# Kernel tuning notes

Measured on AMD Instinct MI355X. Metric: run time of the kernel, lower is better.

The kernel has to match this reference:

```python
import jax, jax.numpy as jnp
import numpy as np

D_MODEL = 1024
NUM_HEADS = 16
DEPTH = D_MODEL // NUM_HEADS
B, S = 2, 2048


def setup_inputs() -> dict:
    key = jax.random.key(0)
    ks = jax.random.split(key, 12)
    scale = 1.0 / np.sqrt(D_MODEL)
    inp = {
        "Q": jax.random.normal(ks[0], (B, S, D_MODEL), jnp.float32),
        "K": jax.random.normal(ks[1], (B, S, D_MODEL), jnp.float32),
        "V": jax.random.normal(ks[2], (B, S, D_MODEL), jnp.float32),
        # causal mask: 1 where attention is disallowed (strictly upper triangular)
        "mask": jnp.triu(jnp.ones((1, 1, S, S), jnp.float32), k=1),
        "Wq": jax.random.normal(ks[3], (D_MODEL, D_MODEL), jnp.float32) * scale,
        "bq": jnp.zeros((D_MODEL,), jnp.float32),
        "Wk": jax.random.normal(ks[4], (D_MODEL, D_MODEL), jnp.float32) * scale,
        "bk": jnp.zeros((D_MODEL,), jnp.float32),
        "Wv": jax.random.normal(ks[5], (D_MODEL, D_MODEL), jnp.float32) * scale,
        "bv": jnp.zeros((D_MODEL,), jnp.float32),
        "Wo": jax.random.normal(ks[6], (D_MODEL, D_MODEL), jnp.float32) * scale,
        "bo": jnp.zeros((D_MODEL,), jnp.float32),
    }
    return inp


def _split_heads(x):
    # [B, S, d_model] -> [B, H, S, depth]
    b, s, _ = x.shape
    return x.reshape(b, s, NUM_HEADS, DEPTH).transpose(0, 2, 1, 3)


def reference(Q, K, V, mask, Wq, bq, Wk, bk, Wv, bv, Wo, bo):
    q = _split_heads(Q @ Wq + bq)  # [B,H,S,depth]
    k = _split_heads(K @ Wk + bk)
    v = _split_heads(V @ Wv + bv)

    scale = 1.0 / jnp.sqrt(jnp.asarray(DEPTH, q.dtype))
    scores = jnp.einsum("bhqd,bhkd->bhqk", q, k) * scale
    scores = scores + mask * (-1e9)
    attn = jax.nn.softmax(scores, axis=-1)  # [B,H,S,S]
    ctx = jnp.einsum("bhqk,bhkd->bhqd", attn, v)

    # combine heads: [B,H,S,depth] -> [B,S,d_model]
    ctx = ctx.transpose(0, 2, 1, 3).reshape(Q.shape[0], -1, D_MODEL)
    out = ctx @ Wo + bo
    return out, attn
```

## Files before the change

### kernel.cpp

```cpp
#include <hip/hip_runtime.h>
#include <hip/hip_bf16.h>
#include <cstdint>
#include <cstddef>


typedef __bf16 bf16x8 __attribute__((ext_vector_type(8)));
typedef float  f32x4  __attribute__((ext_vector_type(4)));
typedef unsigned short u16;
typedef unsigned int   u32;

using gas_p = const __attribute__((address_space(1))) void*;
using las_p = __attribute__((address_space(3))) void*;

static __device__ __forceinline__ u16 f2bf(float x) {
    unsigned u = __builtin_bit_cast(unsigned, x);
    u += 0x7FFFu + ((u >> 16) & 1u);
    return (u16)(u >> 16);
}
static __device__ __forceinline__ u32 pk2(float a, float b) {
    return (u32)f2bf(a) | ((u32)f2bf(b) << 16);
}
static __device__ __forceinline__ f32x4 mfma16(bf16x8 a, bf16x8 b, f32x4 c) {
    return __builtin_amdgcn_mfma_f32_16x16x32_bf16(a, b, c, 0, 0, 0);
}
static __device__ __forceinline__ bf16x8 ldb8(const u16* p) {
    return *reinterpret_cast<const bf16x8*>(p);
}

__global__ __launch_bounds__(256) void transpose_cvt_k(const float* __restrict__ Wq,
                                                       const float* __restrict__ Wk,
                                                       const float* __restrict__ Wv,
                                                       const float* __restrict__ Wo,
                                                       u16* __restrict__ Wt3,
                                                       u16* __restrict__ Wto) {
    const int z = blockIdx.z;
    const float* in = (z == 0) ? Wq : (z == 1) ? Wk : (z == 2) ? Wv : Wo;
    u16* out = (z < 3) ? (Wt3 + (size_t)z * 1048576) : Wto;
    __shared__ float t[32][33];
    const int tx = threadIdx.x, ty = threadIdx.y;
    const int x  = blockIdx.x * 32 + tx;
    const int y0 = blockIdx.y * 32 + ty;
#pragma unroll
    for (int j = 0; j < 32; j += 8)
        t[ty + j][tx] = in[(size_t)(y0 + j) * 1024 + x];
    __syncthreads();
    const int x2 = blockIdx.y * 32 + tx;
    const int y2 = blockIdx.x * 32 + ty;
#pragma unroll
    for (int j = 0; j < 32; j += 8)
        out[(size_t)(y2 + j) * 1024 + x2] = f2bf(t[tx][ty + j]);
}

__global__ __launch_bounds__(256) void gemm_qkv_k(const float* __restrict__ Qf,
                                                  const float* __restrict__ Kf,
                                                  const float* __restrict__ Vf,
                                                  const u16* __restrict__ Wt3,
                                                  const float* __restrict__ bq,
                                                  const float* __restrict__ bk,
                                                  const float* __restrict__ bv,
                                                  u16* __restrict__ qf,
                                                  u16* __restrict__ kf,
                                                  u16* __restrict__ vtf,
                                                  float* __restrict__ attn) {
    constexpr int Kd = 1024;
    constexpr int S = 2048;
    const int z = blockIdx.z;

    if (z == 3) {
        float* attn_h = attn + (size_t)blockIdx.y * S * S;
        const int bx = blockIdx.x;
        const int ro = threadIdx.x >> 4, cc = threadIdx.x & 15;
        const f32x4 zz = {0.f, 0.f, 0.f, 0.f};
        for (int c = 1; c < 32; ++c) {
            float* base = attn_h + (size_t)(bx * 8 * c) * S + c * 64 + cc * 4;
            const int nrows = 8 * c;
            for (int i = ro; i < nrows; i += 16)
                *reinterpret_cast<f32x4*>(base + (size_t)i * S) = zz;
        }
        return;
    }

    const float* Af = (z == 0) ? Qf : (z == 1) ? Kf : Vf;
    const u16* Bt = Wt3 + (size_t)z * 1048576;
    const float* bias = (z == 0) ? bq : (z == 1) ? bk : bv;

    __shared__ __align__(16) u16 As[128 * 64];
    __shared__ __align__(16) u16 Bs[128 * 64];
    const int tid = threadIdx.x;
    const int w = tid >> 6, lane = tid & 63;
    const int g = lane >> 4, lr = lane & 15;
    const int wr = w >> 1, wc = w & 1;
    const int bm = blockIdx.y * 128, bn = blockIdx.x * 128;

    f32x4 acc[4][4];
#pragma unroll
    for (int a = 0; a < 4; ++a)
#pragma unroll
        for (int b = 0; b < 4; ++b) acc[a][b] = f32x4{0.f, 0.f, 0.f, 0.f};

    const int arow = tid >> 3;
    const int ach  = tid & 7;

    for (int kt = 0; kt < Kd; kt += 64) {
        float4 av[8];
#pragma unroll
        for (int it = 0; it < 4; ++it) {
            const float* src = Af + (size_t)(bm + it * 32 + arow) * Kd + kt + ach * 8;
            av[it * 2]     = *reinterpret_cast<const float4*>(src);
            av[it * 2 + 1] = *reinterpret_cast<const float4*>(src + 4);
        }
// ... 101 lines not shown
#pragma unroll
        for (int kk = 0; kk < 2; ++kk) {
            bf16x8 af[4], bfv[4];
#pragma unroll
            for (int mi = 0; mi < 4; ++mi)
                af[mi] = ldb8(As + (wr * 64 + mi * 16 + lr) * 64 + kk * 32 + g * 8);
#pragma unroll
            for (int ni = 0; ni < 4; ++ni)
                bfv[ni] = ldb8(Bs + (wc * 64 + ni * 16 + lr) * 64 + kk * 32 + g * 8);
#pragma unroll
            for (int mi = 0; mi < 4; ++mi)
#pragma unroll
                for (int ni = 0; ni < 4; ++ni)
                    acc[mi][ni] = mfma16(af[mi], bfv[ni], acc[mi][ni]);
        }
        __syncthreads();
    }

#pragma unroll
    for (int ni = 0; ni < 4; ++ni) {
        const int col = bn + wc * 64 + ni * 16 + lr;
        const float bvv = bias[col];
#pragma unroll
        for (int mi = 0; mi < 4; ++mi) {
            const int row0 = bm + wr * 64 + mi * 16 + g * 4;
            f32x4 c = acc[mi][ni];
#pragma unroll
            for (int i = 0; i < 4; ++i)
                dst[(size_t)(row0 + i) * 1024 + col] = c[i] + bvv;
        }
    }
}

__global__ __launch_bounds__(256) void attn_fused_k(const u16* __restrict__ qbuf,
                                                    const u16* __restrict__ kbuf,
                                                    const u16* __restrict__ vtbuf,
                                                    float* __restrict__ attn,
                                                    u16* __restrict__ ctx) {
    constexpr int S = 2048;
    constexpr float SC2 = 0.125f * 1.44269504088896340736f;
    const int a = blockIdx.y * 16 + blockIdx.x;
    const int bh = ((a & 7) << 2) | ((a >> 3) >> 4);
    const int pr = (a >> 3) & 15;
    const int tid = threadIdx.x;
    const int w = tid >> 6, lane = tid & 63, g = lane >> 4, lr = lane & 15;

    const u16* qh = qbuf + (size_t)bh * S * 64;
    const u16* kh = kbuf + (size_t)bh * S * 64;
    const u16* vh = vtbuf + (size_t)bh * 64 * S;
    float* attn_h = attn + (size_t)bh * S * S;

    __shared__ __align__(16) u16 Ks[2][64 * 64];
    __shared__ __align__(16) u16 Vs[2][64 * 64];
    __shared__ __align__(16) u16 P[4][2][16][72];

    const int srow8 = lane >> 3;
    const int scol  = ((lane & 7) ^ srow8) * 8;
    const int swq   = (lr & 7) << 3;
    const int b = bh >> 4, h = bh & 15;

    for (int phase = 0; phase < 2; ++phase) {
        const int j  = phase ? (31 - pr) : pr;
        const int nT = j + 1;
        const int qb = j * 64 + w * 16;
        const int qrow = qb + lr;

        const u16* qp = qh + (size_t)qrow * 64;
        const bf16x8 q0 = ldb8(qp + g * 8);
        const bf16x8 q1 = ldb8(qp + 32 + g * 8);

        const int i0 = w * 2, i1 = w * 2 + 1;
        const int r0 = i0 * 8 + srow8, r1 = i1 * 8 + srow8;

        float lpart = 0.f;
        __builtin_amdgcn_global_load_lds((gas_p)(kh + (size_t)r0 * 64 + scol),
                                         (las_p)(Ks[0] + i0 * 512), 16, 0, 0);
        __builtin_amdgcn_global_load_lds((gas_p)(kh + (size_t)r1 * 64 + scol),
                                         (las_p)(Ks[0] + i1 * 512), 16, 0, 0);
        __syncthreads();
        for (int t = 0; t < nT; ++t) {
            const int cur = t & 1;
            if (t + 1 < nT) {
                const int kr0 = (t + 1) * 64;
                __builtin_amdgcn_global_load_lds(
                    (gas_p)(kh + (size_t)(kr0 + r0) * 64 + scol),
                    (las_p)(Ks[cur ^ 1] + i0 * 512), 16, 0, 0);
                __builtin_amdgcn_global_load_lds(
                    (gas_p)(kh + (size_t)(kr0 + r1) * 64 + scol),
                    (las_p)(Ks[cur ^ 1] + i1 * 512), 16, 0, 0);
                __builtin_amdgcn_sched_barrier(0);
            }
            f32x4 c[4];
#pragma unroll
            for (int n = 0; n < 4; ++n) {
                const u16* kr = Ks[cur] + (n * 16 + lr) * 64;
                f32x4 z4 = {0.f, 0.f, 0.f, 0.f};
                z4   = mfma16(ldb8(kr + ((g * 8) ^ swq)), q0, z4);
                c[n] = mfma16(ldb8(kr + ((32 + g * 8) ^ swq)), q1, z4);
            }
            if (t == j) {
                const int kc = t * 64;
#pragma unroll
                for (int n = 0; n < 4; ++n)
#pragma unroll
                    for (int i = 0; i < 4; ++i) {
                        const int kcol = kc + n * 16 + g * 4 + i;
                        lpart += (kcol <= qrow) ? exp2f(c[n][i] * SC2) : 0.f;
                    }
            } else {
#pragma unroll
                for (int n = 0; n < 4; ++n)
#pragma unroll
                    for (int i = 0; i < 4; ++i)
                        lpart += exp2f(c[n][i] * SC2);
            }
            if (t + 1 < nT) {
                asm volatile("s_waitcnt vmcnt(0)" ::: "memory");
                __builtin_amdgcn_s_barrier();
                __builtin_amdgcn_sched_barrier(0);
            }
        }
        lpart += __shfl_xor(lpart, 16);
        lpart += __shfl_xor(lpart, 32);
        const float mfin = __log2f(lpart);

        f32x4 acc[4];
#pragma unroll
        for (int dn = 0; dn < 4; ++dn) acc[dn] = f32x4{0.f, 0.f, 0.f, 0.f};

        __syncthreads();
        __builtin_amdgcn_global_load_lds((gas_p)(kh + (size_t)r0 * 64 + scol),
                                         (las_p)(Ks[0] + i0 * 512), 16, 0, 0);
        __builtin_amdgcn_global_load_lds((gas_p)(kh + (size_t)r1 * 64 + scol),
                                         (las_p)(Ks[0] + i1 * 512), 16, 0, 0);
        __builtin_amdgcn_global_load_lds((gas_p)(vh + (size_t)r0 * 2048 + scol),
                                         (las_p)(Vs[0] + i0 * 512), 16, 0, 0);
        __builtin_amdgcn_global_load_lds((gas_p)(vh + (size_t)r1 * 2048 + scol),
                                         (las_p)(Vs[0] + i1 * 512), 16, 0, 0);
        __syncthreads();
        for (int t = 0; t < nT; ++t) {
            const int cur = t & 1;
            if (t + 1 < nT) {
                const int kr0 = (t + 1) * 64;
                __builtin_amdgcn_global_load_lds(
                    (gas_p)(kh + (size_t)(kr0 + r0) * 64 + scol),
                    (las_p)(Ks[cur ^ 1] + i0 * 512), 16, 0, 0);
                __builtin_amdgcn_global_load_lds(
                    (gas_p)(kh + (size_t)(kr0 + r1) * 64 + scol),
                    (las_p)(Ks[cur ^ 1] + i1 * 512), 16, 0, 0);
                __builtin_amdgcn_global_load_lds(
                    (gas_p)(vh + (size_t)r0 * 2048 + kr0 + scol),
                    (las_p)(Vs[cur ^ 1] + i0 * 512), 16, 0, 0);
                __builtin_amdgcn_global_load_lds(
                    (gas_p)(vh + (size_t)r1 * 2048 + kr0 + scol),
                    (las_p)(Vs[cur ^ 1] + i1 * 512), 16, 0, 0);
                __builtin_amdgcn_sched_barrier(0);
            }
            const int kc = t * 64;
            f32x4 c[4];
#pragma unroll
            for (int n = 0; n < 4; ++n) {
                const u16* kr = Ks[cur] + (n * 16 + lr) * 64;
                f32x4 z4 = {0.f, 0.f, 0.f, 0.f};
                z4   = mfma16(ldb8(kr + ((g * 8) ^ swq)), q0, z4);
                c[n] = mfma16(ldb8(kr + ((32 + g * 8) ^ swq)), q1, z4);
            }
            const bool diag = (t == j);
#pragma unroll
            for (int n = 0; n < 4; ++n) {
                f32x4 pv;
                if (diag) {
#pragma unroll
                    for (int i = 0; i < 4; ++i) {
                        const int kcol = kc + n * 16 + g * 4 + i;
                        pv[i] = (kcol <= qrow)
                                    ? exp2f(__builtin_fmaf(c[n][i], SC2, -mfin))
                                    : 0.f;
                    }
                } else {
#pragma unroll
                    for (int i = 0; i < 4; ++i)
                        pv[i] = exp2f(__builtin_fmaf(c[n][i], SC2, -mfin));
                }
                *reinterpret_cast<f32x4*>(
                    attn_h + (size_t)qrow * S + kc + n * 16 + g * 4) = pv;
                uint2 pr2;
                pr2.x = pk2(pv[0], pv[1]);
                pr2.y = pk2(pv[2], pv[3]);
                *reinterpret_cast<uint2*>(&P[w][t & 1][lr][n * 16 + g * 4]) = pr2;
            }
            asm volatile("s_waitcnt lgkmcnt(0)" ::: "memory");
            __builtin_amdgcn_sched_barrier(0);
#pragma unroll
            for (int kk = 0; kk < 2; ++kk) {
                const bf16x8 pa = ldb8(&P[w][t & 1][lr][kk * 32 + g * 8]);
#pragma unroll
                for (int dn = 0; dn < 4; ++dn) {
                    const u16* vr = Vs[cur] + (dn * 16 + lr) * 64;
                    acc[dn] = mfma16(pa, ldb8(vr + ((kk * 32 + g * 8) ^ swq)), acc[dn]);
                }
            }
            if (t + 1 < nT) {
                asm volatile("s_waitcnt vmcnt(4)" ::: "memory");
                __builtin_amdgcn_s_barrier();
                __builtin_amdgcn_sched_barrier(0);
            }
        }

#pragma unroll
        for (int dn = 0; dn < 4; ++dn)
#pragma unroll
            for (int i = 0; i < 4; ++i) {
                const size_t row = (size_t)b * S + qb + g * 4 + i;
                ctx[row * 1024 + h * 64 + dn * 16 + lr] = f2bf(acc[dn][i]);
            }
        __syncthreads();
    }
}

extern "C" void kernel_launch(void* const* d_in, const int* in_sizes, int n_in,
                              void* d_out, int out_size, void* d_ws, size_t ws_size,
                              hipStream_t stream) {
    (void)in_sizes; (void)n_in; (void)out_size; (void)ws_size;

    const float* Q  = (const float*)d_in[0];
    const float* K  = (const float*)d_in[1];
    const float* V  = (const float*)d_in[2];
    const float* Wq = (const float*)d_in[4];
    const float* bq = (const float*)d_in[5];
    const float* Wk = (const float*)d_in[6];
    const float* bk = (const float*)d_in[7];
    const float* Wv = (const float*)d_in[8];
    const float* bv = (const float*)d_in[9];
    const float* Wo = (const float*)d_in[10];
    const float* bo = (const float*)d_in[11];

    char* ws = (char*)d_ws;
    u16* Wt3 = (u16*)(ws);
    u16* Wto = (u16*)(ws + ((size_t)6  << 20));
    u16* qf  = (u16*)(ws + ((size_t)8  << 20));
    u16* kf  = (u16*)(ws + ((size_t)16 << 20));
    u16* vtf = (u16*)(ws + ((size_t)24 << 20));
    u16* ctx = (u16*)(ws + ((size_t)32 << 20));

    float* out  = (float*)d_out;
    float* attn = out + (size_t)4096 * 1024;

    transpose_cvt_k<<<dim3(32, 32, 4), dim3(32, 8), 0, stream>>>(Wq, Wk, Wv, Wo, Wt3, Wto);

    gemm_qkv_k<<<dim3(8, 32, 4), 256, 0, stream>>>(Q, K, V, Wt3, bq, bk, bv,
                                                   qf, kf, vtf, attn);

    attn_fused_k<<<dim3(16, 32), 256, 0, stream>>>(qf, kf, vtf, attn, ctx);

    gemm_out_k<<<dim3(8, 32), 256, 0, stream>>>(ctx, Wto, bo, out);
}
```

Measured before the change: 291.8 us.

## Triple-buffer K and V tiles with deeper prefetch and MFMA priority hints

Replaces the separate double-buffered K and V shared arrays with one pool of five tiles. K is triple-buffered in the stats pass and V is triple-buffered in the output pass, so loads are prefetched two tiles ahead. The vmcnt waits are relaxed to match. The per-wave P staging buffer is reduced from two slots to one, and s_setprio is raised around the MFMA blocks. The aim is to hide global-load latency behind compute, at the cost of more LDS per block and possibly lower occupancy. Reusing a single P slot depends on lgkmcnt ordering within each wave.

```diff
diff --git a/kernel.cpp b/kernel.cpp
--- a/kernel.cpp
+++ b/kernel.cpp
@@ -261,9 +261,8 @@
     const u16* vh = vtbuf + (size_t)bh * 64 * S;
     float* attn_h = attn + (size_t)bh * S * S;
 
-    __shared__ __align__(16) u16 Ks[2][64 * 64];
-    __shared__ __align__(16) u16 Vs[2][64 * 64];
-    __shared__ __align__(16) u16 P[4][2][16][72];
+    __shared__ __align__(16) u16 KV[5][64 * 64];
+    __shared__ __align__(16) u16 P[4][16][72];
 
     const int srow8 = lane >> 3;
     const int scol  = ((lane & 7) ^ srow8) * 8;
@@ -285,50 +284,71 @@
 
         float lpart = 0.f;
         __builtin_amdgcn_global_load_lds((gas_p)(kh + (size_t)r0 * 64 + scol),
-                                         (las_p)(Ks[0] + i0 * 512), 16, 0, 0);
+                                         (las_p)(KV[0] + i0 * 512), 16, 0, 0);
         __builtin_amdgcn_global_load_lds((gas_p)(kh + (size_t)r1 * 64 + scol),
-                                         (las_p)(Ks[0] + i1 * 512), 16, 0, 0);
-        __syncthreads();
-        for (int t = 0; t < nT; ++t) {
-            const int cur = t & 1;
-            if (t + 1 < nT) {
-                const int kr0 = (t + 1) * 64;
-                __builtin_amdgcn_global_load_lds(
-                    (gas_p)(kh + (size_t)(kr0 + r0) * 64 + scol),
-                    (las_p)(Ks[cur ^ 1] + i0 * 512), 16, 0, 0);
-                __builtin_amdgcn_global_load_lds(
-                    (gas_p)(kh + (size_t)(kr0 + r1) * 64 + scol),
-                    (las_p)(Ks[cur ^ 1] + i1 * 512), 16, 0, 0);
-                __builtin_amdgcn_sched_barrier(0);
-            }
-            f32x4 c[4];
-#pragma unroll
-            for (int n = 0; n < 4; ++n) {
-                const u16* kr = Ks[cur] + (n * 16 + lr) * 64;
-                f32x4 z4 = {0.f, 0.f, 0.f, 0.f};
-                z4   = mfma16(ldb8(kr + ((g * 8) ^ swq)), q0, z4);
-                c[n] = mfma16(ldb8(kr + ((32 + g * 8) ^ swq)), q1, z4);
-            }
-            if (t == j) {
-                const int kc = t * 64;
-#pragma unroll
-                for (int n = 0; n < 4; ++n)
-#pragma unroll
-                    for (int i = 0; i < 4; ++i) {
-                        const int kcol = kc + n * 16 + g * 4 + i;
-                        lpart += (kcol <= qrow) ? exp2f(c[n][i] * SC2) : 0.f;
+                                         (las_p)(KV[0] + i1 * 512), 16, 0, 0);
+        if (nT > 1) {
+            __builtin_amdgcn_global_load_lds((gas_p)(kh + (size_t)(64 + r0) * 64 + scol),
+                                             (las_p)(KV[1] + i0 * 512), 16, 0, 0);
+            __builtin_amdgcn_global_load_lds((gas_p)(kh + (size_t)(64 + r1) * 64 + scol),
+                                             (las_p)(KV[1] + i1 * 512), 16, 0, 0);
+            asm volatile("s_waitcnt vmcnt(2)" ::: "memory");
+        } else {
+            asm volatile("s_waitcnt vmcnt(0)" ::: "memory");
+        }
+        __builtin_amdgcn_s_barrier();
+        __builtin_amdgcn_sched_barrier(0);
+
+        {
+            int cur = 0, stg = 2;
+            for (int t = 0; t < nT; ++t) {
+                if (t + 2 < nT) {
+                    const int kr0 = (t + 2) * 64;
+                    __builtin_amdgcn_global_load_lds(
+                        (gas_p)(kh + (size_t)(kr0 + r0) * 64 + scol),
+                        (las_p)(KV[stg] + i0 * 512), 16, 0, 0);
+                    __builtin_amdgcn_global_load_lds(
+                        (gas_p)(kh + (size_t)(kr0 + r1) * 64 + scol),
+                        (las_p)(KV[stg] + i1 * 512), 16, 0, 0);
+                    __builtin_amdgcn_sched_barrier(0);
+                }
+                f32x4 c[4];
+                __builtin_amdgcn_s_setprio(1);
+#pragma unroll
+                for (int n = 0; n < 4; ++n) {
+                    const u16* kr = KV[cur] + (n * 16 + lr) * 64;
+                    f32x4 z4 = {0.f, 0.f, 0.f, 0.f};
+                    z4   = mfma16(ldb8(kr + ((g * 8) ^ swq)), q0, z4);
+                    c[n] = mfma16(ldb8(kr + ((32 + g * 8) ^ swq)), q1, z4);
+                }
+                __builtin_amdgcn_s_setprio(0);
+                if (t == j) {
+                    const int kc = t * 64;
+#pragma unroll
+                    for (int n = 0; n < 4; ++n)
+#pragma unroll
+                        for (int i = 0; i < 4; ++i) {
+                            const int kcol = kc + n * 16 + g * 4 + i;
+                            lpart += (kcol <= qrow) ? exp2f(c[n][i] * SC2) : 0.f;
+                        }
+                } else {
+#pragma unroll
+                    for (int n = 0; n < 4; ++n)
+#pragma unroll
+                        for (int i = 0; i < 4; ++i)
+                            lpart += exp2f(c[n][i] * SC2);
+                }
+                if (t + 1 < nT) {
+                    if (t + 2 < nT) {
+                        asm volatile("s_waitcnt vmcnt(2)" ::: "memory");
+                    } else {
+                        asm volatile("s_waitcnt vmcnt(0)" ::: "memory");
                     }
-            } else {
-#pragma unroll
-                for (int n = 0; n < 4; ++n)
-#pragma unroll
-                    for (int i = 0; i < 4; ++i)
-                        lpart += exp2f(c[n][i] * SC2);
-            }
-            if (t + 1 < nT) {
-                asm volatile("s_waitcnt vmcnt(0)" ::: "memory");
-                __builtin_amdgcn_s_barrier();
-                __builtin_amdgcn_sched_barrier(0);
+                    __builtin_amdgcn_s_barrier();
+                    __builtin_amdgcn_sched_barrier(0);
+                }
+                cur = (cur == 2) ? 0 : cur + 1;
+                stg = (stg == 2) ? 0 : stg + 1;
             }
         }
         lpart += __shfl_xor(lpart, 16);
@@ -341,80 +361,108 @@
 
         __syncthreads();
         __builtin_amdgcn_global_load_lds((gas_p)(kh + (size_t)r0 * 64 + scol),
-                                         (las_p)(Ks[0] + i0 * 512), 16, 0, 0);
+                                         (las_p)(KV[0] + i0 * 512), 16, 0, 0);
         __builtin_amdgcn_global_load_lds((gas_p)(kh + (size_t)r1 * 64 + scol),
-                                         (las_p)(Ks[0] + i1 * 512), 16, 0, 0);
+                                         (las_p)(KV[0] + i1 * 512), 16, 0, 0);
         __builtin_amdgcn_global_load_lds((gas_p)(vh + (size_t)r0 * 2048 + scol),
-                                         (las_p)(Vs[0] + i0 * 512), 16, 0, 0);
+                                         (las_p)(KV[2] + i0 * 512), 16, 0, 0);
         __builtin_amdgcn_global_load_lds((gas_p)(vh + (size_t)r1 * 2048 + scol),
-                                         (las_p)(Vs[0] + i1 * 512), 16, 0, 0);
-        __syncthreads();
-        for (int t = 0; t < nT; ++t) {
-            const int cur = t & 1;
-            if (t + 1 < nT) {
-                const int kr0 = (t + 1) * 64;
-                __builtin_amdgcn_global_load_lds(
-                    (gas_p)(kh + (size_t)(kr0 + r0) * 64 + scol),
-                    (las_p)(Ks[cur ^ 1] + i0 * 512), 16, 0, 0);
-                __builtin_amdgcn_global_load_lds(
-                    (gas_p)(kh + (size_t)(kr0 + r1) * 64 + scol),
-                    (las_p)(Ks[cur ^ 1] + i1 * 512), 16, 0, 0);
-                __builtin_amdgcn_global_load_lds(
-                    (gas_p)(vh + (size_t)r0 * 2048 + kr0 + scol),
-                    (las_p)(Vs[cur ^ 1] + i0 * 512), 16, 0, 0);
-                __builtin_amdgcn_global_load_lds(
-                    (gas_p)(vh + (size_t)r1 * 2048 + kr0 + scol),
-                    (las_p)(Vs[cur ^ 1] + i1 * 512), 16, 0, 0);
+                                         (las_p)(KV[2] + i1 * 512), 16, 0, 0);
+        if (nT > 1) {
+            __builtin_amdgcn_global_load_lds((gas_p)(vh + (size_t)r0 * 2048 + 64 + scol),
+                                             (las_p)(KV[3] + i0 * 512), 16, 0, 0);
+            __builtin_amdgcn_global_load_lds((gas_p)(vh + (size_t)r1 * 2048 + 64 + scol),
+                                             (las_p)(KV[3] + i1 * 512), 16, 0, 0);
+            asm volatile("s_waitcnt vmcnt(2)" ::: "memory");
+        } else {
+            asm volatile("s_waitcnt vmcnt(0)" ::: "memory");
+        }
+        __builtin_amdgcn_s_barrier();
+        __builtin_amdgcn_sched_barrier(0);
+
+        {
+            int vcur = 2, vstg = 4;
+            for (int t = 0; t < nT; ++t) {
+                const int kcur = t & 1;
+                if (t + 1 < nT) {
+                    const int kr0 = (t + 1) * 64;
+                    __builtin_amdgcn_global_load_lds(
+                        (gas_p)(kh + (size_t)(kr0 + r0) * 64 + scol),
+                        (las_p)(KV[kcur ^ 1] + i0 * 512), 16, 0, 0);
+                    __builtin_amdgcn_global_load_lds(
+                        (gas_p)(kh + (size_t)(kr0 + r1) * 64 + scol),
+                        (las_p)(KV[kcur ^ 1] + i1 * 512), 16, 0, 0);
+                }
+                if (t + 2 < nT) {
+                    const int vc0 = (t + 2) * 64;
+                    __builtin_amdgcn_global_load_lds(
+                        (gas_p)(vh + (size_t)r0 * 2048 + vc0 + scol),
+                        (las_p)(KV[vstg] + i0 * 512), 16, 0, 0);
+                    __builtin_amdgcn_global_load_lds(
+                        (gas_p)(vh + (size_t)r1 * 2048 + vc0 + scol),
+                        (las_p)(KV[vstg] + i1 * 512), 16, 0, 0);
+                }
                 __builtin_amdgcn_sched_barrier(0);
-            }
-            const int kc = t * 64;
-            f32x4 c[4];
-#pragma unroll
-            for (int n = 0; n < 4; ++n) {
-                const u16* kr = Ks[cur] + (n * 16 + lr) * 64;
-                f32x4 z4 = {0.f, 0.f, 0.f, 0.f};
-                z4   = mfma16(ldb8(kr + ((g * 8) ^ swq)), q0, z4);
-                c[n] = mfma16(ldb8(kr + ((32 + g * 8) ^ swq)), q1, z4);
-            }
-            const bool diag = (t == j);
-#pragma unroll
-            for (int n = 0; n < 4; ++n) {
-                f32x4 pv;
-                if (diag) {
-#pragma unroll
-                    for (int i = 0; i < 4; ++i) {
-                        const int kcol = kc + n * 16 + g * 4 + i;
-                        pv[i] = (kcol <= qrow)
-                                    ? exp2f(__builtin_fmaf(c[n][i], SC2, -mfin))
-                                    : 0.f;
+
+                const int kc = t * 64;
+                f32x4 c[4];
+                __builtin_amdgcn_s_setprio(1);
+#pragma unroll
+                for (int n = 0; n < 4; ++n) {
+                    const u16* kr = KV[kcur] + (n * 16 + lr) * 64;
+                    f32x4 z4 = {0.f, 0.f, 0.f, 0.f};
+                    z4   = mfma16(ldb8(kr + ((g * 8) ^ swq)), q0, z4);
+                    c[n] = mfma16(ldb8(kr + ((32 + g * 8) ^ swq)), q1, z4);
+                }
+                __builtin_amdgcn_s_setprio(0);
+                const bool diag = (t == j);
+#pragma unroll
+                for (int n = 0; n < 4; ++n) {
+                    f32x4 pv;
+                    if (diag) {
+#pragma unroll
+                        for (int i = 0; i < 4; ++i) {
+                            const int kcol = kc + n * 16 + g * 4 + i;
+                            pv[i] = (kcol <= qrow)
+                                        ? exp2f(__builtin_fmaf(c[n][i], SC2, -mfin))
+                                        : 0.f;
+                        }
+                    } else {
+#pragma unroll
+                        for (int i = 0; i < 4; ++i)
+                            pv[i] = exp2f(__builtin_fmaf(c[n][i], SC2, -mfin));
                     }
-                } else {
-#pragma unroll
-                    for (int i = 0; i < 4; ++i)
-                        pv[i] = exp2f(__builtin_fmaf(c[n][i], SC2, -mfin));
-                }
-                *reinterpret_cast<f32x4*>(
-                    attn_h + (size_t)qrow * S + kc + n * 16 + g * 4) = pv;
-                uint2 pr2;
-                pr2.x = pk2(pv[0], pv[1]);
-                pr2.y = pk2(pv[2], pv[3]);
-                *reinterpret_cast<uint2*>(&P[w][t & 1][lr][n * 16 + g * 4]) = pr2;
-            }
-            asm volatile("s_waitcnt lgkmcnt(0)" ::: "memory");
-            __builtin_amdgcn_sched_barrier(0);
-#pragma unroll
-            for (int kk = 0; kk < 2; ++kk) {
-                const bf16x8 pa = ldb8(&P[w][t & 1][lr][kk * 32 + g * 8]);
-#pragma unroll
-                for (int dn = 0; dn < 4; ++dn) {
-                    const u16* vr = Vs[cur] + (dn * 16 + lr) * 64;
-                    acc[dn] = mfma16(pa, ldb8(vr + ((kk * 32 + g * 8) ^ swq)), acc[dn]);
-                }
-            }
-            if (t + 1 < nT) {
-                asm volatile("s_waitcnt vmcnt(4)" ::: "memory");
-                __builtin_amdgcn_s_barrier();
+                    *reinterpret_cast<f32x4*>(
+                        attn_h + (size_t)qrow * S + kc + n * 16 + g * 4) = pv;
+                    uint2 pr2;
+                    pr2.x = pk2(pv[0], pv[1]);
+                    pr2.y = pk2(pv[2], pv[3]);
+                    *reinterpret_cast<uint2*>(&P[w][lr][n * 16 + g * 4]) = pr2;
+                }
+                asm volatile("s_waitcnt lgkmcnt(0)" ::: "memory");
                 __builtin_amdgcn_sched_barrier(0);
+                __builtin_amdgcn_s_setprio(1);
+#pragma unroll
+                for (int kk = 0; kk < 2; ++kk) {
+                    const bf16x8 pa = ldb8(&P[w][lr][kk * 32 + g * 8]);
+#pragma unroll
+                    for (int dn = 0; dn < 4; ++dn) {
+                        const u16* vr = KV[vcur] + (dn * 16 + lr) * 64;
+                        acc[dn] = mfma16(pa, ldb8(vr + ((kk * 32 + g * 8) ^ swq)), acc[dn]);
+                    }
+                }
+                __builtin_amdgcn_s_setprio(0);
+                if (t + 1 < nT) {
+                    if (t + 2 < nT) {
+                        asm volatile("s_waitcnt vmcnt(6)" ::: "memory");
+                    } else {
+                        asm volatile("s_waitcnt vmcnt(4)" ::: "memory");
+                    }
+                    __builtin_amdgcn_s_barrier();
+                    __builtin_amdgcn_sched_barrier(0);
+                }
+                vcur = (vcur == 4) ? 2 : vcur + 1;
+                vstg = (vstg == 4) ? 2 : vstg + 1;
             }
         }
 
```

New measurement: 293.7 us (median of 4 runs). Within noise of the previous version (+0.7%).

## Split paired causal query tiles into separate blocks with swizzled P buffer

Applied to the files above, without the earlier changes.

Each attention block previously handled two query tiles (j and 31-j) in sequence for load balance. Now each block handles one tile and the grid doubles to 1024 blocks, with a remapped block-to-tile order that interleaves long and short tiles. It also sets launch_bounds occupancy to 4, adds s_setprio around the MFMA sections, and replaces the padded double-buffered P staging with a single XOR-swizzled buffer to cut LDS use. The goal is more parallelism and occupancy, at the cost of per-block imbalance, which now relies on the hardware scheduler.

```diff
diff --git a/kernel.cpp b/kernel.cpp
--- a/kernel.cpp
+++ b/kernel.cpp
@@ -41,14 +41,14 @@
     const int x  = blockIdx.x * 32 + tx;
     const int y0 = blockIdx.y * 32 + ty;
 #pragma unroll
-    for (int j = 0; j < 32; j += 8)
-        t[ty + j][tx] = in[(size_t)(y0 + j) * 1024 + x];
+    for (int jj = 0; jj < 32; jj += 8)
+        t[ty + jj][tx] = in[(size_t)(y0 + jj) * 1024 + x];
     __syncthreads();
     const int x2 = blockIdx.y * 32 + tx;
     const int y2 = blockIdx.x * 32 + ty;
 #pragma unroll
-    for (int j = 0; j < 32; j += 8)
-        out[(size_t)(y2 + j) * 1024 + x2] = f2bf(t[tx][ty + j]);
+    for (int jj = 0; jj < 32; jj += 8)
+        out[(size_t)(y2 + jj) * 1024 + x2] = f2bf(t[tx][ty + jj]);
 }
 
 __global__ __launch_bounds__(256) void gemm_qkv_k(const float* __restrict__ Qf,
@@ -243,16 +243,22 @@
     }
 }
 
-__global__ __launch_bounds__(256) void attn_fused_k(const u16* __restrict__ qbuf,
-                                                    const u16* __restrict__ kbuf,
-                                                    const u16* __restrict__ vtbuf,
-                                                    float* __restrict__ attn,
-                                                    u16* __restrict__ ctx) {
+__global__ __launch_bounds__(256, 4) void attn_fused_k(const u16* __restrict__ qbuf,
+                                                       const u16* __restrict__ kbuf,
+                                                       const u16* __restrict__ vtbuf,
+                                                       float* __restrict__ attn,
+                                                       u16* __restrict__ ctx) {
     constexpr int S = 2048;
     constexpr float SC2 = 0.125f * 1.44269504088896340736f;
-    const int a = blockIdx.y * 16 + blockIdx.x;
-    const int bh = ((a & 7) << 2) | ((a >> 3) >> 4);
-    const int pr = (a >> 3) & 15;
+    const int lid = blockIdx.x + (blockIdx.y << 5);
+    const int b4  = lid >> 8;
+    const int c8  = lid & 255;
+    const int x0  = c8 & 31;
+    const int xb  = (b4 & 2) ? ((x0 + 8) & 31) : x0;
+    const int j   = (b4 & 1) ? (31 - xb) : xb;
+    const int bh  = (c8 >> 5) | (b4 << 3);
+    const int nT  = j + 1;
+
     const int tid = threadIdx.x;
     const int w = tid >> 6, lane = tid & 63, g = lane >> 4, lr = lane & 15;
 
@@ -263,170 +269,181 @@
 
     __shared__ __align__(16) u16 Ks[2][64 * 64];
     __shared__ __align__(16) u16 Vs[2][64 * 64];
-    __shared__ __align__(16) u16 P[4][2][16][72];
+    __shared__ __align__(16) u16 Pb[4][16 * 64];
 
     const int srow8 = lane >> 3;
     const int scol  = ((lane & 7) ^ srow8) * 8;
     const int swq   = (lr & 7) << 3;
+    const int lrr   = lr & 7;
     const int b = bh >> 4, h = bh & 15;
 
-    for (int phase = 0; phase < 2; ++phase) {
-        const int j  = phase ? (31 - pr) : pr;
-        const int nT = j + 1;
-        const int qb = j * 64 + w * 16;
-        const int qrow = qb + lr;
-
-        const u16* qp = qh + (size_t)qrow * 64;
-        const bf16x8 q0 = ldb8(qp + g * 8);
-        const bf16x8 q1 = ldb8(qp + 32 + g * 8);
-
-        const int i0 = w * 2, i1 = w * 2 + 1;
-        const int r0 = i0 * 8 + srow8, r1 = i1 * 8 + srow8;
-
-        float lpart = 0.f;
-        __builtin_amdgcn_global_load_lds((gas_p)(kh + (size_t)r0 * 64 + scol),
-                                         (las_p)(Ks[0] + i0 * 512), 16, 0, 0);
-        __builtin_amdgcn_global_load_lds((gas_p)(kh + (size_t)r1 * 64 + scol),
-                                         (las_p)(Ks[0] + i1 * 512), 16, 0, 0);
-        __syncthreads();
-        for (int t = 0; t < nT; ++t) {
-            const int cur = t & 1;
-            if (t + 1 < nT) {
-                const int kr0 = (t + 1) * 64;
-                __builtin_amdgcn_global_load_lds(
-                    (gas_p)(kh + (size_t)(kr0 + r0) * 64 + scol),
-                    (las_p)(Ks[cur ^ 1] + i0 * 512), 16, 0, 0);
-                __builtin_amdgcn_global_load_lds(
-                    (gas_p)(kh + (size_t)(kr0 + r1) * 64 + scol),
-                    (las_p)(Ks[cur ^ 1] + i1 * 512), 16, 0, 0);
-                __builtin_amdgcn_sched_barrier(0);
+    const int qb = j * 64 + w * 16;
+    const int qrow = qb + lr;
+
+    const u16* qp = qh + (size_t)qrow * 64;
+    const bf16x8 q0 = ldb8(qp + g * 8);
+    const bf16x8 q1 = ldb8(qp + 32 + g * 8);
+
+    const int i0 = w * 2, i1 = w * 2 + 1;
+    const int r0 = i0 * 8 + srow8, r1 = i1 * 8 + srow8;
+    u16* Pw = &Pb[w][0];
+
+    float lpart = 0.f;
+    __builtin_amdgcn_global_load_lds((gas_p)(kh + (size_t)r0 * 64 + scol),
+                                     (las_p)(Ks[0] + i0 * 512), 16, 0, 0);
+    __builtin_amdgcn_global_load_lds((gas_p)(kh + (size_t)r1 * 64 + scol),
+                                     (las_p)(Ks[0] + i1 * 512), 16, 0, 0);
+    asm volatile("s_waitcnt vmcnt(0)" ::: "memory");
+    __builtin_amdgcn_s_barrier();
+    __builtin_amdgcn_sched_barrier(0);
+
+    for (int t = 0; t < nT; ++t) {
+        const int cur = t & 1;
+        if (t + 1 < nT) {
+            const int kr0 = (t + 1) * 64;
+            __builtin_amdgcn_global_load_lds(
+                (gas_p)(kh + (size_t)(kr0 + r0) * 64 + scol),
+                (las_p)(Ks[cur ^ 1] + i0 * 512), 16, 0, 0);
+            __builtin_amdgcn_global_load_lds(
+                (gas_p)(kh + (size_t)(kr0 + r1) * 64 + scol),
+                (las_p)(Ks[cur ^ 1] + i1 * 512), 16, 0, 0);
+            __builtin_amdgcn_sched_barrier(0);
+        }
+        f32x4 c[4];
+        __builtin_amdgcn_s_setprio(1);
+#pragma unroll
+        for (int n = 0; n < 4; ++n) {
+            const u16* kr = Ks[cur] + (n * 16 + lr) * 64;
+            f32x4 z4 = {0.f, 0.f, 0.f, 0.f};
+            z4   = mfma16(ldb8(kr + ((g * 8) ^ swq)), q0, z4);
+            c[n] = mfma16(ldb8(kr + ((32 + g * 8) ^ swq)), q1, z4);
+        }
+        __builtin_amdgcn_s_setprio(0);
+        if (t == j) {
+            const int kc = t * 64;
+#pragma unroll
+            for (int n = 0; n < 4; ++n)
+#pragma unroll
+                for (int i = 0; i < 4; ++i) {
+                    const int kcol = kc + n * 16 + g * 4 + i;
+                    lpart += (kcol <= qrow) ? exp2f(c[n][i] * SC2) : 0.f;
+                }
+        } else {
+#pragma unroll
+            for (int n = 0; n < 4; ++n)
+#pragma unroll
+                for (int i = 0; i < 4; ++i)
+                    lpart += exp2f(c[n][i] * SC2);
+        }
+        if (t + 1 < nT) {
+            asm volatile("s_waitcnt vmcnt(0)" ::: "memory");
+            __builtin_amdgcn_s_barrier();
+            __builtin_amdgcn_sched_barrier(0);
+        }
+    }
+    lpart += __shfl_xor(lpart, 16);
+    lpart += __shfl_xor(lpart, 32);
+    const float mfin = __log2f(lpart);
+
+    f32x4 acc[4];
+#pragma unroll
+    for (int dn = 0; dn < 4; ++dn) acc[dn] = f32x4{0.f, 0.f, 0.f, 0.f};
+
+    __syncthreads();
+    __builtin_amdgcn_global_load_lds((gas_p)(kh + (size_t)r0 * 64 + scol),
+                                     (las_p)(Ks[0] + i0 * 512), 16, 0, 0);
+    __builtin_amdgcn_global_load_lds((gas_p)(kh + (size_t)r1 * 64 + scol),
+                                     (las_p)(Ks[0] + i1 * 512), 16, 0, 0);
+    __builtin_amdgcn_global_load_lds((gas_p)(vh + (size_t)r0 * 2048 + scol),
+                                     (las_p)(Vs[0] + i0 * 512), 16, 0, 0);
+    __builtin_amdgcn_global_load_lds((gas_p)(vh + (size_t)r1 * 2048 + scol),
+                                     (las_p)(Vs[0] + i1 * 512), 16, 0, 0);
+    asm volatile("s_waitcnt vmcnt(0)" ::: "memory");
+    __builtin_amdgcn_s_barrier();
+    __builtin_amdgcn_sched_barrier(0);
+
+    for (int t = 0; t < nT; ++t) {
+        const int cur = t & 1;
+        if (t + 1 < nT) {
+            const int kr0 = (t + 1) * 64;
+            __builtin_amdgcn_global_load_lds(
+                (gas_p)(kh + (size_t)(kr0 + r0) * 64 + scol),
+                (las_p)(Ks[cur ^ 1] + i0 * 512), 16, 0, 0);
+            __builtin_amdgcn_global_load_lds(
+                (gas_p)(kh + (size_t)(kr0 + r1) * 64 + scol),
+                (las_p)(Ks[cur ^ 1] + i1 * 512), 16, 0, 0);
+            __builtin_amdgcn_global_load_lds(
+                (gas_p)(vh + (size_t)r0 * 2048 + kr0 + scol),
+                (las_p)(Vs[cur ^ 1] + i0 * 512), 16, 0, 0);
+            __builtin_amdgcn_global_load_lds(
+                (gas_p)(vh + (size_t)r1 * 2048 + kr0 + scol),
+                (las_p)(Vs[cur ^ 1] + i1 * 512), 16, 0, 0);
+            __builtin_amdgcn_sched_barrier(0);
+        }
+        const int kc = t * 64;
+        f32x4 c[4];
+        __builtin_amdgcn_s_setprio(1);
+#pragma unroll
+        for (int n = 0; n < 4; ++n) {
+            const u16* kr = Ks[cur] + (n * 16 + lr) * 64;
+            f32x4 z4 = {0.f, 0.f, 0.f, 0.f};
+            z4   = mfma16(ldb8(kr + ((g * 8) ^ swq)), q0, z4);
+            c[n] = mfma16(ldb8(kr + ((32 + g * 8) ^ swq)), q1, z4);
+        }
+        __builtin_amdgcn_s_setprio(0);
+        const bool diag = (t == j);
+#pragma unroll
+        for (int n = 0; n < 4; ++n) {
+            f32x4 pv;
+            if (diag) {
+#pragma unroll
+                for (int i = 0; i < 4; ++i) {
+                    const int kcol = kc + n * 16 + g * 4 + i;
+                    pv[i] = (kcol <= qrow)
+                                ? exp2f(__builtin_fmaf(c[n][i], SC2, -mfin))
+                                : 0.f;
+                }
+            } else {
+#pragma unroll
+                for (int i = 0; i < 4; ++i)
+                    pv[i] = exp2f(__builtin_fmaf(c[n][i], SC2, -mfin));
             }
-            f32x4 c[4];
-#pragma unroll
-            for (int n = 0; n < 4; ++n) {
-                const u16* kr = Ks[cur] + (n * 16 + lr) * 64;
-                f32x4 z4 = {0.f, 0.f, 0.f, 0.f};
-                z4   = mfma16(ldb8(kr + ((g * 8) ^ swq)), q0, z4);
-                c[n] = mfma16(ldb8(kr + ((32 + g * 8) ^ swq)), q1, z4);
+            uint2 pr2;
+            pr2.x = pk2(pv[0], pv[1]);
+            pr2.y = pk2(pv[2], pv[3]);
+            const int pwo = lr * 64 + ((((n << 1) | (g >> 1)) ^ lrr) << 3)
+                          + ((g & 1) << 2);
+            *reinterpret_cast<uint2*>(Pw + pwo) = pr2;
+            *reinterpret_cast<f32x4*>(
+                attn_h + (size_t)qrow * S + kc + n * 16 + g * 4) = pv;
+        }
+        asm volatile("s_waitcnt lgkmcnt(0)" ::: "memory");
+        __builtin_amdgcn_sched_barrier(0);
+        __builtin_amdgcn_s_setprio(1);
+#pragma unroll
+        for (int kk = 0; kk < 2; ++kk) {
+            const bf16x8 pa = ldb8(Pw + lr * 64 + ((((kk << 2) | g) ^ lrr) << 3));
+#pragma unroll
+            for (int dn = 0; dn < 4; ++dn) {
+                const u16* vr = Vs[cur] + (dn * 16 + lr) * 64;
+                acc[dn] = mfma16(pa, ldb8(vr + ((kk * 32 + g * 8) ^ swq)), acc[dn]);
             }
-            if (t == j) {
-                const int kc = t * 64;
-#pragma unroll
-                for (int n = 0; n < 4; ++n)
-#pragma unroll
-                    for (int i = 0; i < 4; ++i) {
-                        const int kcol = kc + n * 16 + g * 4 + i;
-                        lpart += (kcol <= qrow) ? exp2f(c[n][i] * SC2) : 0.f;
-                    }
-            } else {
-#pragma unroll
-                for (int n = 0; n < 4; ++n)
-#pragma unroll
-                    for (int i = 0; i < 4; ++i)
-                        lpart += exp2f(c[n][i] * SC2);
-            }
-            if (t + 1 < nT) {
-                asm volatile("s_waitcnt vmcnt(0)" ::: "memory");
-                __builtin_amdgcn_s_barrier();
-                __builtin_amdgcn_sched_barrier(0);
-            }
-        }
-        lpart += __shfl_xor(lpart, 16);
-        lpart += __shfl_xor(lpart, 32);
-        const float mfin = __log2f(lpart);
-
-        f32x4 acc[4];
-#pragma unroll
-        for (int dn = 0; dn < 4; ++dn) acc[dn] = f32x4{0.f, 0.f, 0.f, 0.f};
-
-        __syncthreads();
-        __builtin_amdgcn_global_load_lds((gas_p)(kh + (size_t)r0 * 64 + scol),
-                                         (las_p)(Ks[0] + i0 * 512), 16, 0, 0);
-        __builtin_amdgcn_global_load_lds((gas_p)(kh + (size_t)r1 * 64 + scol),
-                                         (las_p)(Ks[0] + i1 * 512), 16, 0, 0);
-        __builtin_amdgcn_global_load_lds((gas_p)(vh + (size_t)r0 * 2048 + scol),
-                                         (las_p)(Vs[0] + i0 * 512), 16, 0, 0);
-        __builtin_amdgcn_global_load_lds((gas_p)(vh + (size_t)r1 * 2048 + scol),
-                                         (las_p)(Vs[0] + i1 * 512), 16, 0, 0);
-        __syncthreads();
-        for (int t = 0; t < nT; ++t) {
-            const int cur = t & 1;
-            if (t + 1 < nT) {
-                const int kr0 = (t + 1) * 64;
-                __builtin_amdgcn_global_load_lds(
-                    (gas_p)(kh + (size_t)(kr0 + r0) * 64 + scol),
-                    (las_p)(Ks[cur ^ 1] + i0 * 512), 16, 0, 0);
-                __builtin_amdgcn_global_load_lds(
-                    (gas_p)(kh + (size_t)(kr0 + r1) * 64 + scol),
-                    (las_p)(Ks[cur ^ 1] + i1 * 512), 16, 0, 0);
-                __builtin_amdgcn_global_load_lds(
-                    (gas_p)(vh + (size_t)r0 * 2048 + kr0 + scol),
-                    (las_p)(Vs[cur ^ 1] + i0 * 512), 16, 0, 0);
-                __builtin_amdgcn_global_load_lds(
-                    (gas_p)(vh + (size_t)r1 * 2048 + kr0 + scol),
-                    (las_p)(Vs[cur ^ 1] + i1 * 512), 16, 0, 0);
-                __builtin_amdgcn_sched_barrier(0);
-            }
-            const int kc = t * 64;
-            f32x4 c[4];
-#pragma unroll
-            for (int n = 0; n < 4; ++n) {
-                const u16* kr = Ks[cur] + (n * 16 + lr) * 64;
-                f32x4 z4 = {0.f, 0.f, 0.f, 0.f};
-                z4   = mfma16(ldb8(kr + ((g * 8) ^ swq)), q0, z4);
-                c[n] = mfma16(ldb8(kr + ((32 + g * 8) ^ swq)), q1, z4);
-            }
-            const bool diag = (t == j);
-#pragma unroll
-            for (int n = 0; n < 4; ++n) {
-                f32x4 pv;
-                if (diag) {
-#pragma unroll
-                    for (int i = 0; i < 4; ++i) {
-                        const int kcol = kc + n * 16 + g * 4 + i;
-                        pv[i] = (kcol <= qrow)
-                                    ? exp2f(__builtin_fmaf(c[n][i], SC2, -mfin))
-                                    : 0.f;
-                    }
-                } else {
-#pragma unroll
-                    for (int i = 0; i < 4; ++i)
-                        pv[i] = exp2f(__builtin_fmaf(c[n][i], SC2, -mfin));
-                }
-                *reinterpret_cast<f32x4*>(
-                    attn_h + (size_t)qrow * S + kc + n * 16 + g * 4) = pv;
-                uint2 pr2;
-                pr2.x = pk2(pv[0], pv[1]);
-                pr2.y = pk2(pv[2], pv[3]);
-                *reinterpret_cast<uint2*>(&P[w][t & 1][lr][n * 16 + g * 4]) = pr2;
-            }
-            asm volatile("s_waitcnt lgkmcnt(0)" ::: "memory");
+        }
+        __builtin_amdgcn_s_setprio(0);
+        if (t + 1 < nT) {
+            asm volatile("s_waitcnt vmcnt(4)" ::: "memory");
+            __builtin_amdgcn_s_barrier();
             __builtin_amdgcn_sched_barrier(0);
-#pragma unroll
-            for (int kk = 0; kk < 2; ++kk) {
-                const bf16x8 pa = ldb8(&P[w][t & 1][lr][kk * 32 + g * 8]);
-#pragma unroll
-                for (int dn = 0; dn < 4; ++dn) {
-                    const u16* vr = Vs[cur] + (dn * 16 + lr) * 64;
-                    acc[dn] = mfma16(pa, ldb8(vr + ((kk * 32 + g * 8) ^ swq)), acc[dn]);
-                }
-            }
-            if (t + 1 < nT) {
-                asm volatile("s_waitcnt vmcnt(4)" ::: "memory");
-                __builtin_amdgcn_s_barrier();
-                __builtin_amdgcn_sched_barrier(0);
-            }
-        }
-
-#pragma unroll
-        for (int dn = 0; dn < 4; ++dn)
-#pragma unroll
-            for (int i = 0; i < 4; ++i) {
-                const size_t row = (size_t)b * S + qb + g * 4 + i;
-                ctx[row * 1024 + h * 64 + dn * 16 + lr] = f2bf(acc[dn][i]);
-            }
-        __syncthreads();
-    }
+        }
+    }
+
+#pragma unroll
+    for (int dn = 0; dn < 4; ++dn)
+#pragma unroll
+        for (int i = 0; i < 4; ++i) {
+            const size_t row = (size_t)b * S + qb + g * 4 + i;
+            ctx[row * 1024 + h * 64 + dn * 16 + lr] = f2bf(acc[dn][i]);
+        }
 }
 
 extern "C" void kernel_launch(void* const* d_in, const int* in_sizes, int n_in,
@@ -462,7 +479,7 @@
     gemm_qkv_k<<<dim3(8, 32, 4), 256, 0, stream>>>(Q, K, V, Wt3, bq, bk, bv,
                                                    qf, kf, vtf, attn);
 
-    attn_fused_k<<<dim3(16, 32), 256, 0, stream>>>(qf, kf, vtf, attn, ctx);
+    attn_fused_k<<<dim3(32, 32), 256, 0, stream>>>(qf, kf, vtf, attn, ctx);
 
     gemm_out_k<<<dim3(8, 32), 256, 0, stream>>>(ctx, Wto, bo, out);
 }
```

New measurement: 301.3 us. +3.3%, slower.

## Split attention key range across wave pairs and drop LDS K/V staging

Applied to the files above, without the earlier changes.

Restructures the fused attention kernel so each block handles half the query rows of a paired tile, with two waves splitting each row's key tiles and combining softmax denominators and partial context sums through shared memory. K and V tiles are now read directly from global memory instead of being double-buffered in LDS, and the grid is doubled with a launch-bounds occupancy hint. Attention-probability writes and the zero fill of the masked region use nontemporal stores to avoid polluting cache. This raises parallelism and occupancy but loses LDS reuse of K/V across waves and adds a cross-wave reduction and extra syncs.

```diff
diff --git a/kernel.cpp b/kernel.cpp
--- a/kernel.cpp
+++ b/kernel.cpp
@@ -41,14 +41,14 @@
     const int x  = blockIdx.x * 32 + tx;
     const int y0 = blockIdx.y * 32 + ty;
 #pragma unroll
-    for (int j = 0; j < 32; j += 8)
-        t[ty + j][tx] = in[(size_t)(y0 + j) * 1024 + x];
+    for (int jj = 0; jj < 32; jj += 8)
+        t[ty + jj][tx] = in[(size_t)(y0 + jj) * 1024 + x];
     __syncthreads();
     const int x2 = blockIdx.y * 32 + tx;
     const int y2 = blockIdx.x * 32 + ty;
 #pragma unroll
-    for (int j = 0; j < 32; j += 8)
-        out[(size_t)(y2 + j) * 1024 + x2] = f2bf(t[tx][ty + j]);
+    for (int jj = 0; jj < 32; jj += 8)
+        out[(size_t)(y2 + jj) * 1024 + x2] = f2bf(t[tx][ty + jj]);
 }
 
 __global__ __launch_bounds__(256) void gemm_qkv_k(const float* __restrict__ Qf,
@@ -75,7 +75,8 @@
             float* base = attn_h + (size_t)(bx * 8 * c) * S + c * 64 + cc * 4;
             const int nrows = 8 * c;
             for (int i = ro; i < nrows; i += 16)
-                *reinterpret_cast<f32x4*>(base + (size_t)i * S) = zz;
+                __builtin_nontemporal_store(zz,
+                    reinterpret_cast<f32x4*>(base + (size_t)i * S));
         }
         return;
     }
@@ -243,140 +244,114 @@
     }
 }
 
-__global__ __launch_bounds__(256) void attn_fused_k(const u16* __restrict__ qbuf,
-                                                    const u16* __restrict__ kbuf,
-                                                    const u16* __restrict__ vtbuf,
-                                                    float* __restrict__ attn,
-                                                    u16* __restrict__ ctx) {
+__global__ __launch_bounds__(256, 4) void attn_fused_k(const u16* __restrict__ qbuf,
+                                                       const u16* __restrict__ kbuf,
+                                                       const u16* __restrict__ vtbuf,
+                                                       float* __restrict__ attn,
+                                                       u16* __restrict__ ctx) {
     constexpr int S = 2048;
     constexpr float SC2 = 0.125f * 1.44269504088896340736f;
-    const int a = blockIdx.y * 16 + blockIdx.x;
-    const int bh = ((a & 7) << 2) | ((a >> 3) >> 4);
-    const int pr = (a >> 3) & 15;
+    const int bh = blockIdx.x;
+    const int u  = blockIdx.y;
+    const int jp = u >> 1, qsel = u & 1;
     const int tid = threadIdx.x;
     const int w = tid >> 6, lane = tid & 63, g = lane >> 4, lr = lane & 15;
+    const int tw = w >> 1;
+    const int kh_ = w & 1;
+    const int q  = qsel * 2 + tw;
 
     const u16* qh = qbuf + (size_t)bh * S * 64;
     const u16* kh = kbuf + (size_t)bh * S * 64;
     const u16* vh = vtbuf + (size_t)bh * 64 * S;
     float* attn_h = attn + (size_t)bh * S * S;
 
-    __shared__ __align__(16) u16 Ks[2][64 * 64];
-    __shared__ __align__(16) u16 Vs[2][64 * 64];
-    __shared__ __align__(16) u16 P[4][2][16][72];
-
-    const int srow8 = lane >> 3;
-    const int scol  = ((lane & 7) ^ srow8) * 8;
-    const int swq   = (lr & 7) << 3;
+    __shared__ __align__(16) u16 P[4][16][72];
+    __shared__ float ACCL[4][16][64];
+    __shared__ float2 Lx[4][16];
+
+    const int jv[2] = {jp, 31 - jp};
     const int b = bh >> 4, h = bh & 15;
 
-    for (int phase = 0; phase < 2; ++phase) {
-        const int j  = phase ? (31 - pr) : pr;
-        const int nT = j + 1;
-        const int qb = j * 64 + w * 16;
-        const int qrow = qb + lr;
-
-        const u16* qp = qh + (size_t)qrow * 64;
-        const bf16x8 q0 = ldb8(qp + g * 8);
-        const bf16x8 q1 = ldb8(qp + 32 + g * 8);
-
-        const int i0 = w * 2, i1 = w * 2 + 1;
-        const int r0 = i0 * 8 + srow8, r1 = i1 * 8 + srow8;
-
-        float lpart = 0.f;
-        __builtin_amdgcn_global_load_lds((gas_p)(kh + (size_t)r0 * 64 + scol),
-                                         (las_p)(Ks[0] + i0 * 512), 16, 0, 0);
-        __builtin_amdgcn_global_load_lds((gas_p)(kh + (size_t)r1 * 64 + scol),
-                                         (las_p)(Ks[0] + i1 * 512), 16, 0, 0);
-        __syncthreads();
-        for (int t = 0; t < nT; ++t) {
-            const int cur = t & 1;
-            if (t + 1 < nT) {
-                const int kr0 = (t + 1) * 64;
-                __builtin_amdgcn_global_load_lds(
-                    (gas_p)(kh + (size_t)(kr0 + r0) * 64 + scol),
-                    (las_p)(Ks[cur ^ 1] + i0 * 512), 16, 0, 0);
-                __builtin_amdgcn_global_load_lds(
-                    (gas_p)(kh + (size_t)(kr0 + r1) * 64 + scol),
-                    (las_p)(Ks[cur ^ 1] + i1 * 512), 16, 0, 0);
-                __builtin_amdgcn_sched_barrier(0);
-            }
+    int t0a[2], t1a[2];
+#pragma unroll
+    for (int p = 0; p < 2; ++p) {
+        const int nT = jv[p] + 1;
+        const int hh = nT >> 1;
+        t0a[p] = kh_ ? hh : 0;
+        t1a[p] = kh_ ? nT : hh;
+    }
+
+    bf16x8 q0[2], q1[2];
+    int qrow[2];
+#pragma unroll
+    for (int p = 0; p < 2; ++p) {
+        qrow[p] = jv[p] * 64 + q * 16 + lr;
+        const u16* qp = qh + (size_t)qrow[p] * 64;
+        q0[p] = ldb8(qp + g * 8);
+        q1[p] = ldb8(qp + 32 + g * 8);
+    }
+
+    float lp[2] = {0.f, 0.f};
+#pragma unroll
+    for (int p = 0; p < 2; ++p) {
+        const int jc = jv[p];
+        for (int t = t0a[p]; t < t1a[p]; ++t) {
+            const u16* kt_ = kh + (size_t)t * 64 * 64;
             f32x4 c[4];
 #pragma unroll
             for (int n = 0; n < 4; ++n) {
-                const u16* kr = Ks[cur] + (n * 16 + lr) * 64;
+                const u16* kr = kt_ + (size_t)(n * 16 + lr) * 64;
                 f32x4 z4 = {0.f, 0.f, 0.f, 0.f};
-                z4   = mfma16(ldb8(kr + ((g * 8) ^ swq)), q0, z4);
-                c[n] = mfma16(ldb8(kr + ((32 + g * 8) ^ swq)), q1, z4);
-            }
-            if (t == j) {
+                z4   = mfma16(ldb8(kr + g * 8), q0[p], z4);
+                c[n] = mfma16(ldb8(kr + 32 + g * 8), q1[p], z4);
+            }
+            if (t == jc) {
                 const int kc = t * 64;
 #pragma unroll
                 for (int n = 0; n < 4; ++n)
 #pragma unroll
                     for (int i = 0; i < 4; ++i) {
                         const int kcol = kc + n * 16 + g * 4 + i;
-                        lpart += (kcol <= qrow) ? exp2f(c[n][i] * SC2) : 0.f;
+                        lp[p] += (kcol <= qrow[p]) ? exp2f(c[n][i] * SC2) : 0.f;
                     }
             } else {
 #pragma unroll
                 for (int n = 0; n < 4; ++n)
 #pragma unroll
                     for (int i = 0; i < 4; ++i)
-                        lpart += exp2f(c[n][i] * SC2);
-            }
-            if (t + 1 < nT) {
-                asm volatile("s_waitcnt vmcnt(0)" ::: "memory");
-                __builtin_amdgcn_s_barrier();
-                __builtin_amdgcn_sched_barrier(0);
-            }
-        }
-        lpart += __shfl_xor(lpart, 16);
-        lpart += __shfl_xor(lpart, 32);
-        const float mfin = __log2f(lpart);
-
+                        lp[p] += exp2f(c[n][i] * SC2);
+            }
+        }
+        lp[p] += __shfl_xor(lp[p], 16);
+        lp[p] += __shfl_xor(lp[p], 32);
+    }
+    Lx[w][lr] = make_float2(lp[0], lp[1]);
+    __syncthreads();
+    const float2 lo = Lx[w ^ 1][lr];
+    const float mf0 = __log2f(lp[0] + lo.x);
+    const float mf1 = __log2f(lp[1] + lo.y);
+    const float mfv[2] = {mf0, mf1};
+
+#pragma unroll
+    for (int p = 0; p < 2; ++p) {
+        const int jc = jv[p];
+        const float mfin = mfv[p];
         f32x4 acc[4];
 #pragma unroll
         for (int dn = 0; dn < 4; ++dn) acc[dn] = f32x4{0.f, 0.f, 0.f, 0.f};
 
-        __syncthreads();
-        __builtin_amdgcn_global_load_lds((gas_p)(kh + (size_t)r0 * 64 + scol),
-                                         (las_p)(Ks[0] + i0 * 512), 16, 0, 0);
-        __builtin_amdgcn_global_load_lds((gas_p)(kh + (size_t)r1 * 64 + scol),
-                                         (las_p)(Ks[0] + i1 * 512), 16, 0, 0);
-        __builtin_amdgcn_global_load_lds((gas_p)(vh + (size_t)r0 * 2048 + scol),
-                                         (las_p)(Vs[0] + i0 * 512), 16, 0, 0);
-        __builtin_amdgcn_global_load_lds((gas_p)(vh + (size_t)r1 * 2048 + scol),
-                                         (las_p)(Vs[0] + i1 * 512), 16, 0, 0);
-        __syncthreads();
-        for (int t = 0; t < nT; ++t) {
-            const int cur = t & 1;
-            if (t + 1 < nT) {
-                const int kr0 = (t + 1) * 64;
-                __builtin_amdgcn_global_load_lds(
-                    (gas_p)(kh + (size_t)(kr0 + r0) * 64 + scol),
-                    (las_p)(Ks[cur ^ 1] + i0 * 512), 16, 0, 0);
-                __builtin_amdgcn_global_load_lds(
-                    (gas_p)(kh + (size_t)(kr0 + r1) * 64 + scol),
-                    (las_p)(Ks[cur ^ 1] + i1 * 512), 16, 0, 0);
-                __builtin_amdgcn_global_load_lds(
-                    (gas_p)(vh + (size_t)r0 * 2048 + kr0 + scol),
-                    (las_p)(Vs[cur ^ 1] + i0 * 512), 16, 0, 0);
-                __builtin_amdgcn_global_load_lds(
-                    (gas_p)(vh + (size_t)r1 * 2048 + kr0 + scol),
-                    (las_p)(Vs[cur ^ 1] + i1 * 512), 16, 0, 0);
-                __builtin_amdgcn_sched_barrier(0);
-            }
+        for (int t = t0a[p]; t < t1a[p]; ++t) {
             const int kc = t * 64;
+            const u16* kt_ = kh + (size_t)kc * 64;
             f32x4 c[4];
 #pragma unroll
             for (int n = 0; n < 4; ++n) {
-                const u16* kr = Ks[cur] + (n * 16 + lr) * 64;
+                const u16* kr = kt_ + (size_t)(n * 16 + lr) * 64;
                 f32x4 z4 = {0.f, 0.f, 0.f, 0.f};
-                z4   = mfma16(ldb8(kr + ((g * 8) ^ swq)), q0, z4);
-                c[n] = mfma16(ldb8(kr + ((32 + g * 8) ^ swq)), q1, z4);
-            }
-            const bool diag = (t == j);
+                z4   = mfma16(ldb8(kr + g * 8), q0[p], z4);
+                c[n] = mfma16(ldb8(kr + 32 + g * 8), q1[p], z4);
+            }
+            const bool diag = (t == jc);
 #pragma unroll
             for (int n = 0; n < 4; ++n) {
                 f32x4 pv;
@@ -384,7 +359,7 @@
 #pragma unroll
                     for (int i = 0; i < 4; ++i) {
                         const int kcol = kc + n * 16 + g * 4 + i;
-                        pv[i] = (kcol <= qrow)
+                        pv[i] = (kcol <= qrow[p])
                                     ? exp2f(__builtin_fmaf(c[n][i], SC2, -mfin))
                                     : 0.f;
                     }
@@ -393,39 +368,47 @@
                     for (int i = 0; i < 4; ++i)
                         pv[i] = exp2f(__builtin_fmaf(c[n][i], SC2, -mfin));
                 }
-                *reinterpret_cast<f32x4*>(
-                    attn_h + (size_t)qrow * S + kc + n * 16 + g * 4) = pv;
+                __builtin_nontemporal_store(pv,
+                    reinterpret_cast<f32x4*>(
+                        attn_h + (size_t)qrow[p] * S + kc + n * 16 + g * 4));
                 uint2 pr2;
                 pr2.x = pk2(pv[0], pv[1]);
                 pr2.y = pk2(pv[2], pv[3]);
-                *reinterpret_cast<uint2*>(&P[w][t & 1][lr][n * 16 + g * 4]) = pr2;
+                *reinterpret_cast<uint2*>(&P[w][lr][n * 16 + g * 4]) = pr2;
             }
             asm volatile("s_waitcnt lgkmcnt(0)" ::: "memory");
             __builtin_amdgcn_sched_barrier(0);
 #pragma unroll
             for (int kk = 0; kk < 2; ++kk) {
-                const bf16x8 pa = ldb8(&P[w][t & 1][lr][kk * 32 + g * 8]);
+                const bf16x8 pa = ldb8(&P[w][lr][kk * 32 + g * 8]);
 #pragma unroll
                 for (int dn = 0; dn < 4; ++dn) {
-                    const u16* vr = Vs[cur] + (dn * 16 + lr) * 64;
-                    acc[dn] = mfma16(pa, ldb8(vr + ((kk * 32 + g * 8) ^ swq)), acc[dn]);
+                    const u16* vr = vh + (size_t)(dn * 16 + lr) * S + kc + kk * 32 + g * 8;
+                    acc[dn] = mfma16(pa, ldb8(vr), acc[dn]);
                 }
             }
-            if (t + 1 < nT) {
-                asm volatile("s_waitcnt vmcnt(4)" ::: "memory");
-                __builtin_amdgcn_s_barrier();
-                __builtin_amdgcn_sched_barrier(0);
-            }
-        }
-
-#pragma unroll
-        for (int dn = 0; dn < 4; ++dn)
-#pragma unroll
-            for (int i = 0; i < 4; ++i) {
-                const size_t row = (size_t)b * S + qb + g * 4 + i;
-                ctx[row * 1024 + h * 64 + dn * 16 + lr] = f2bf(acc[dn][i]);
-            }
+        }
+
+        const int slot = tw + 2 * p;
+        if (kh_ == 0) {
+#pragma unroll
+            for (int dn = 0; dn < 4; ++dn)
+#pragma unroll
+                for (int i = 0; i < 4; ++i)
+                    ACCL[slot][g * 4 + i][dn * 16 + lr] = acc[dn][i];
+        }
         __syncthreads();
+        if (kh_ == 1) {
+            const int qb = jv[p] * 64 + q * 16;
+#pragma unroll
+            for (int dn = 0; dn < 4; ++dn)
+#pragma unroll
+                for (int i = 0; i < 4; ++i) {
+                    const float vsum = acc[dn][i] + ACCL[slot][g * 4 + i][dn * 16 + lr];
+                    const size_t row = (size_t)b * S + qb + g * 4 + i;
+                    ctx[row * 1024 + h * 64 + dn * 16 + lr] = f2bf(vsum);
+                }
+        }
     }
 }
 
@@ -462,7 +445,7 @@
     gemm_qkv_k<<<dim3(8, 32, 4), 256, 0, stream>>>(Q, K, V, Wt3, bq, bk, bv,
                                                    qf, kf, vtf, attn);
 
-    attn_fused_k<<<dim3(16, 32), 256, 0, stream>>>(qf, kf, vtf, attn, ctx);
+    attn_fused_k<<<dim3(32, 32), 256, 0, stream>>>(qf, kf, vtf, attn, ctx);
 
     gemm_out_k<<<dim3(8, 32), 256, 0, stream>>>(ctx, Wto, bo, out);
 }
```

Measured after the change: 343.4 us. +17.7%, slower.
